# Performance work log

Hardware: AMD Instinct MI355X
Metric: run time of the kernel (lower is better)

## Reference

```python
import jax, jax.numpy as jnp
import numpy as np

B, N_SIDE, S = 64, 40, 512
N = N_SIDE * N_SIDE          # 1600 grid points (fl_feature_dims [1,40,40])
EMB = 10                     # embedding_dim
GDIM = 8                     # lie('homography').dim
WIDTH = 128
C1 = 20                      # first-layer output channels


def _embed(x, emb_dim):
    # sinusoidal embedding of each scalar coordinate: [..., D] -> [..., D*emb_dim]
    freqs = 2.0 ** jnp.arange(emb_dim // 2, dtype=x.dtype)
    ang = x[..., None] * freqs                       # [..., D, emb/2]
    e = jnp.concatenate([jnp.sin(ang), jnp.cos(ang)], axis=-1)  # [..., D, emb]
    return e.reshape(x.shape[:-1] + (x.shape[-1] * emb_dim,))


def _glorot(key, shape):
    fan_in = shape[0]
    return jax.random.normal(key, shape, dtype=jnp.float32) / np.sqrt(fan_in)


def setup_inputs() -> dict:
    key = jax.random.key(0)
    ks = jax.random.split(key, 16)
    inp = {
        'data':   jax.random.normal(ks[0], (B, N, 1), dtype=jnp.float32),
        'v0':     jax.random.normal(ks[1], (S, GDIM), dtype=jnp.float32),
        'v_last': jax.random.normal(ks[2], (S, GDIM), dtype=jnp.float32),
        # FirstLayer filter MLP: 2*EMB -> 20 -> 20 -> 1*C1
        'fl_w1': _glorot(ks[3], (2 * EMB, 20)), 'fl_b1': jnp.zeros((20,), jnp.float32),
        'fl_w2': _glorot(ks[4], (20, 20)),      'fl_b2': jnp.zeros((20,), jnp.float32),
        'fl_w3': _glorot(ks[5], (20, C1)),      'fl_b3': jnp.zeros((C1,), jnp.float32),
        # Hidden FilterMLP: EMB*GDIM=80 -> WIDTH -> C1*WIDTH
        's_w1': _glorot(ks[6], (EMB * GDIM, WIDTH)), 's_b1': jnp.zeros((WIDTH,), jnp.float32),
        's_w2': _glorot(ks[7], (WIDTH, C1 * WIDTH)), 's_b2': jnp.zeros((C1 * WIDTH,), jnp.float32),
        'fc1_w': _glorot(ks[8], (WIDTH, WIDTH)), 'fc1_b': jnp.zeros((WIDTH,), jnp.float32),
        'fc2_w': _glorot(ks[9], (WIDTH, WIDTH)), 'fc2_b': jnp.zeros((WIDTH,), jnp.float32),
        'pool_w': _glorot(ks[10], (WIDTH, 10)),  'pool_b': jnp.zeros((10,), jnp.float32),
    }
    return inp


def reference(data, v0, v_last, fl_w1, fl_b1, fl_w2, fl_b2, fl_w3, fl_b3,
              s_w1, s_b1, s_w2, s_b2, fc1_w, fc1_b, fc2_w, fc2_b, pool_w, pool_b):
    silu = jax.nn.silu
    # pixel grid in [-1,1]^2, homogeneous coords [N,3]
    lin = jnp.linspace(-1.0, 1.0, N_SIDE, dtype=data.dtype)
    xx, yy = jnp.meshgrid(lin, lin, indexing='ij')
    coords = jnp.stack([xx.ravel(), yy.ravel()], axis=-1)           # [N,2]
    xh = jnp.concatenate([coords, jnp.ones((N, 1), data.dtype)], -1)  # [N,3]
    # homography matrices: identity + small perturbation from 8 group params
    pert = jnp.concatenate([0.1 * v_last, jnp.zeros((S, 1), data.dtype)], -1).reshape(S, 3, 3)
    H = jnp.eye(3, dtype=data.dtype) + pert                          # [S,3,3]
    y = jnp.einsum('sij,nj->sni', H, xh)                             # [S,N,3]
    t = y[..., :2] / y[..., 2:3]                                     # projective action [S,N,2]
    # continuous-kernel first layer: filters generated by MLP on embedded coords
    e1 = _embed(t, EMB)                                              # [S,N,20]
    h = silu(e1 @ fl_w1 + fl_b1)
    h = silu(h @ fl_w2 + fl_b2)
    filt1 = h @ fl_w3 + fl_b3                                        # [S,N,C1]
    z = jnp.einsum('bn,sno->bso', data[:, :, 0], filt1) / N          # [B,S,C1]
    z = silu(z)
    # hidden FilterMLP on group samples v0 -> per-sample filters [S,C1,WIDTH]
    v0e = _embed(v0, EMB)                                            # [S,80]
    h2 = silu(v0e @ s_w1 + s_b1)                                     # [S,WIDTH]
    filt2 = (h2 @ s_w2 + s_b2).reshape(S, C1, WIDTH)
    # (1/S) * sum over group-sample and channel axes of broadcast product
    z = jnp.einsum('bsc,scw->bw', z, filt2) / S                      # [B,WIDTH]
    z = silu(z @ fc1_w + fc1_b) + z
    z = silu(z @ fc2_w + fc2_b) + z
    return z @ pool_w + pool_b                                       # [B,10]
```

## Files before the change

### kernel.cpp

```cpp
#include <hip/hip_runtime.h>

#define N_PTS 1600
#define NSIDE 40
#define SNUM  512
#define BNUM  64
#define C1D   20
#define WID   128

typedef _Float16 h8  __attribute__((ext_vector_type(8)));
typedef _Float16 h4  __attribute__((ext_vector_type(4)));
typedef __fp16   h2v __attribute__((ext_vector_type(2)));
typedef float    f4  __attribute__((ext_vector_type(4)));

__device__ __forceinline__ float silu_f(float x){
    return x * __builtin_amdgcn_rcpf(1.f + __expf(-x));
}
__device__ __forceinline__ void fma4(float4& a, float s, const float4 w){
    a.x += s*w.x; a.y += s*w.y; a.z += s*w.z; a.w += s*w.w;
}

__global__ __launch_bounds__(256) void ka_prep(
    const float* __restrict__ data, const float* __restrict__ v0,
    const float* __restrict__ s_w1, const float* __restrict__ s_b1,
    const float* __restrict__ s_w2, const float* __restrict__ s_b2,
    const float* __restrict__ w1, const float* __restrict__ b1,
    const float* __restrict__ w2, const float* __restrict__ b2,
    const float* __restrict__ w3, const float* __restrict__ b3,
    _Float16* __restrict__ dataA, float* __restrict__ f2g,
    _Float16* __restrict__ wPackA, float* __restrict__ bPackA,
    float* __restrict__ out2g)
{
    const int t  = threadIdx.x;
    const int bx = blockIdx.x;
    if (bx == 370) {
        const float* wsrc[3] = { w1, w2, w3 };
        const float* bsrc[3] = { b1, b2, b3 };
        for (int v = t; v < 3072; v += 256) {
            const int l = v >> 10, rem = v & 1023;
            const int cout = rem >> 5, cin = rem & 31;
            float x = 0.f;
            if (cout < 20 && cin < 20) x = wsrc[l][cin * 20 + cout];
            wPackA[v] = (_Float16)x;
        }
        if (t < 96) {
            const int l = t >> 5, cout = t & 31;
            bPackA[t] = (cout < 20) ? bsrc[l][cout] : 0.f;
        }
        for (int v = t; v < 8192; v += 256) out2g[v] = 0.f;
        return;
    }
    if (bx >= 320) {
        const int o  = (bx - 320) * 256 + t;
        const int L  = o & 63, cm = o >> 6;
        const int mt = cm & 3, ch = cm >> 2;
        const int b  = mt * 16 + (L & 15);
        const int nb = ch * 32 + (L >> 4) * 8;
        const float* src = data + b * N_PTS + nb;
        h8 v;
        #pragma unroll
        for (int j = 0; j < 8; j++) v[j] = (_Float16)src[j];
        *(h8*)(dataA + (size_t)o * 8) = v;
        return;
    }
    const int st  = bx / 10, ct = bx - st * 10;
    const int s0  = st * 16;
    const int col = ct * 256 + t;
    __shared__ __align__(16) float h2t[128][20];
    __shared__ __align__(16) float svt[16][8][10];

    if (t < 128) {
        const int ss = t >> 3, d = t & 7;
        const float val = v0[(s0 + ss) * 8 + d];
        float sv, cv;
        __sincosf(val, &sv, &cv);
        #pragma unroll
        for (int k = 0; k < 5; k++) {
            svt[ss][d][k]     = sv;
            svt[ss][d][5 + k] = cv;
            const float ns = 2.f * sv * cv;
            const float nc = 1.f - 2.f * sv * sv;
            sv = ns; cv = nc;
        }
    }
    __syncthreads();

    {
        const int j  = t & 127;
        const int sh = t >> 7;
        float hacc[8];
        const float bias1 = s_b1[j];
        #pragma unroll
        for (int u = 0; u < 8; u++) hacc[u] = bias1;
        for (int d = 0; d < 8; d++) {
            #pragma unroll
            for (int kk = 0; kk < 10; kk++) {
                const float wv = s_w1[(d * 10 + kk) * WID + j];
                #pragma unroll
                for (int u = 0; u < 8; u++)
                    hacc[u] += svt[sh * 8 + u][d][kk] * wv;
            }
        }
        #pragma unroll
        for (int u = 0; u < 8; u++) h2t[j][sh * 8 + u] = silu_f(hacc[u]);
    }
    __syncthreads();

    float4 acc[4];
    #pragma unroll
    for (int qq = 0; qq < 4; qq++) acc[qq] = make_float4(0.f, 0.f, 0.f, 0.f);
    #pragma unroll 4
    for (int i = 0; i < 128; i++) {
        const float wv = s_w2[i * 2560 + col];
        const float4* hh = (const float4*)&h2t[i][0];
        #pragma unroll
        for (int qq = 0; qq < 4; qq++) fma4(acc[qq], wv, hh[qq]);
    }
    const float bias = s_b2[col];
    const float* af = (const float*)acc;
    #pragma unroll
    for (int ss = 0; ss < 16; ss++)
        f2g[(s0 + ss) * 2560 + col] = af[ss] + bias;
}

__device__ __forceinline__ void embed_coord(
    int n, float hA, float hB, float hC, float h6, float h7, float h8c,
    h2v e5[5])
{
    const int i = n / NSIDE;
    const int j = n - i * NSIDE;
    const float x = -1.f + (float)i * (2.f/39.f);
    const float y = -1.f + (float)j * (2.f/39.f);
    const float yc = hA*x + hB*y + hC;
    const float y2 = h6*x + h7*y + h8c;
    const float tc = yc * __builtin_amdgcn_rcpf(y2);
    float e[10];
    float sv, cv;
    __sincosf(tc, &sv, &cv);
    #pragma unroll
    for (int k = 0; k < 5; k++) {
        e[k] = sv; e[5+k] = cv;
        const float ns = 2.f*sv*cv, nc = 1.f - 2.f*sv*sv; sv = ns; cv = nc;
    }
    #pragma unroll
    for (int k = 0; k < 5; k++)
        e5[k] = __builtin_amdgcn_cvt_pkrtz(e[2*k], e[2*k+1]);
}

#define ASTRIDE 40

__global__ __launch_bounds__(512, 8) void k1_filt_z(
    const _Float16* __restrict__ dataA, const float* __restrict__ v_last,
    const _Float16* __restrict__ wPackA, const float* __restrict__ bPackA,
    float* __restrict__ zpart)
{
    const int s    = blockIdx.x & 511;
    const int half = blockIdx.x >> 9;
    const int nb0  = half * 800;
    const int t    = threadIdx.x;
    const int lane = t & 63;
    const int w    = t >> 6;
    const int q    = lane >> 4;
    const int l15  = lane & 15;
    const int mtbase = (w & 1) * 2;
    const int kcs    = w >> 1;
    const int ep   = lane >> 1;
    const int ec   = lane & 1;
    const int erow = w*16 + ep + ((ep >> 4) * 112);

    __shared__ __align__(16) unsigned char pool[21504];
    __shared__ __align__(16) _Float16 filtB[20 * 264];
    __shared__ __align__(16) _Float16 wlds[3072];
    __shared__ __align__(16) float    blds[96];
    _Float16* act = (_Float16*)pool;
    float*    red = (float*)pool;

    for (int v = t; v < 1536; v += 512)
        ((unsigned int*)wlds)[v] = ((const unsigned int*)wPackA)[v];
    if (t < 96) blds[t] = bPackA[t];

    float Hm[9];
    #pragma unroll
    for (int k = 0; k < 9; k++) Hm[k] = (k == 0 || k == 4 || k == 8) ? 1.f : 0.f;
    #pragma unroll
    for (int k = 0; k < 8; k++) Hm[k] += 0.1f * v_last[s*8 + k];
    const float hA = ec ? Hm[3] : Hm[0];
    const float hB = ec ? Hm[4] : Hm[1];
    const float hC = ec ? Hm[5] : Hm[2];

    f4 zacc[2][2];
    #pragma unroll
    for (int mi = 0; mi < 2; mi++) { zacc[mi][0] = (f4)(0.f); zacc[mi][1] = (f4)(0.f); }
    const f4 zero4 = (f4)(0.f);

    if (ec == 0) {
        unsigned long long* pz = (unsigned long long*)(act + erow*ASTRIDE + 20);
        pz[0] = 0ull; pz[1] = 0ull; pz[2] = 0ull;
    }

    __syncthreads();

    for (int base = 0; base < 800; base += 256) {
        const int tn = min(256, 800 - base);

        if (erow < tn) {
            h2v e5[5];
            embed_coord(nb0 + base + erow, hA, hB, hC, Hm[6], Hm[7], Hm[8], e5);
            #pragma unroll
            for (int k = 0; k < 5; k++)
                *(h2v*)(act + erow*ASTRIDE + ec*10 + 2*k) = e5[k];
        }

        const int nmt = tn >> 4;
        #pragma unroll
        for (int l = 0; l < 3; l++) {
            const h8 wf0 = *(const h8*)(wlds + ((l*2+0)*16 + l15) * 32 + q*8);
            const h8 wf1 = *(const h8*)(wlds + ((l*2+1)*16 + l15) * 32 + q*8);
            const float b0 = blds[(l*2+0)*16 + l15];
            const float b1 = blds[(l*2+1)*16 + l15];
            for (int mt = w; mt < nmt; mt += 8) {
                const int r0 = mt * 16;
                const h8 af = *(const h8*)(act + (r0 + l15)*ASTRIDE + q*8);
                f4 D0 = __builtin_amdgcn_mfma_f32_16x16x32_f16(af, wf0, zero4, 0, 0, 0);
                f4 D1 = __builtin_amdgcn_mfma_f32_16x16x32_f16(af, wf1, zero4, 0, 0, 0);
                if (l < 2) {
                    #pragma unroll
                    for (int r = 0; r < 4; r++) {
                        const int p = r0 + q*4 + r;
                        act[p*ASTRIDE + l15] = (_Float16)silu_f(D0[r] + b0);
                        if (l15 < 4)
                            act[p*ASTRIDE + 16 + l15] = (_Float16)silu_f(D1[r] + b1);
                    }
                } else {
                    h4 p0, p1;
                    #pragma unroll
                    for (int r = 0; r < 4; r++) {
                        p0[r] = (_Float16)(D0[r] + b0);
                        p1[r] = (_Float16)(D1[r] + b1);
                    }
                    *(h4*)(filtB + l15*264 + r0 + q*4) = p0;
                    if (l15 < 4)
                        *(h4*)(filtB + (16 + l15)*264 + r0 + q*4) = p1;
                }
            }
        }
        __syncthreads();

        const int nkc = tn >> 5;
        const int r1row = (l15 < 4) ? (16 + l15) : 0;
        #pragma unroll
        for (int kk = 0; kk < 2; kk++) {
            const int kc = kcs + kk*4;
            if (kc < nkc) {
                const int gchunk = ((nb0 + base) >> 5) + kc;
                const h8 bf0 = *(const h8*)(filtB + l15  *264 + kc*32 + q*8);
                const h8 bf1 = *(const h8*)(filtB + r1row*264 + kc*32 + q*8);
                #pragma unroll
                for (int mi = 0; mi < 2; mi++) {
                    const int mt = mtbase + mi;
                    const h8 afz = *(const h8*)(dataA + ((size_t)(gchunk*4 + mt)*64 + lane)*8);
                    zacc[mi][0] = __builtin_amdgcn_mfma_f32_16x16x32_f16(afz, bf0, zacc[mi][0], 0, 0, 0);
                    zacc[mi][1] = __builtin_amdgcn_mfma_f32_16x16x32_f16(afz, bf1, zacc[mi][1], 0, 0, 0);
                }
            }
        }
        __syncthreads();
    }

    #pragma unroll
    for (int mi = 0; mi < 2; mi++) {
        #pragma unroll
        for (int r = 0; r < 4; r++) {
            const int bl = mi*16 + q*4 + r;
            red[(w*32 + bl)*21 + l15] = zacc[mi][0][r];
            if (l15 < 4) red[(w*32 + bl)*21 + 16 + l15] = zacc[mi][1][r];
        }
    }
    __syncthreads();
    for (int v = t; v < 1280; v += 512) {
        const int c = v >> 6, b = v & 63;
        const int mts = b >> 5, bl = b & 31;
        const float sum = red[((mts    )*32 + bl)*21 + c]
                        + red[((mts + 2)*32 + bl)*21 + c]
                        + red[((mts + 4)*32 + bl)*21 + c]
                        + red[((mts + 6)*32 + bl)*21 + c];
        zpart[(half*512 + s)*1280 + v] = sum;
    }
}

__global__ __launch_bounds__(256) void k2_contract(
    const float* __restrict__ zg, const float* __restrict__ f2g,
    float* __restrict__ out2g)
{
    const int blk = blockIdx.x;
    const int sg  = blk >> 1;
    const int wh  = blk & 1;
    const int s0  = sg * 4;
    const int w0  = wh * 64;
    const int t   = threadIdx.x;
    __shared__ __align__(16) float zl[4*1280];
    __shared__ __align__(16) float fl[4*20*64];
    #pragma unroll
    for (int sp = 0; sp < 4; sp++) {
        const int srow = (s0 + sp) * 1280;
        for (int r = t; r < 1280; r += 256) {
            const float a0 = zg[srow + r];
            const float a1 = zg[512*1280 + srow + r];
            zl[sp*1280 + r] = silu_f((a0 + a1) * (1.f / (float)N_PTS));
        }
        for (int u = t; u < 1280; u += 256) {
            const int c = u >> 6, ww = u & 63;
            fl[sp*1280 + u] = f2g[(s0 + sp)*2560 + c*128 + w0 + ww];
        }
    }
    __syncthreads();
    const int ww = t & 63, bh = t >> 6;
    float4 acc[4];
    #pragma unroll
    for (int qq = 0; qq < 4; qq++) acc[qq] = make_float4(0.f, 0.f, 0.f, 0.f);
    #pragma unroll 4
    for (int sc = 0; sc < 80; sc++) {
        const float f = fl[sc * 64 + ww];
        const float4* zz = (const float4*)&zl[sc * 64 + bh * 16];
        #pragma unroll
        for (int qq = 0; qq < 4; qq++) fma4(acc[qq], f, zz[qq]);
    }
    const float* af = (const float*)acc;
    #pragma unroll
    for (int idx = 0; idx < 16; idx++) {
        const int b = bh * 16 + idx;
        atomicAdd(&out2g[b * 128 + w0 + ww], af[idx]);
    }
}

__global__ __launch_bounds__(128) void k3_tail(
    const float* __restrict__ out2g,
    const float* __restrict__ fc1w, const float* __restrict__ fc1b,
    const float* __restrict__ fc2w, const float* __restrict__ fc2b,
    const float* __restrict__ pw,   const float* __restrict__ pb,
    float* __restrict__ out)
{
    const int b = blockIdx.x, t = threadIdx.x;
    __shared__ float zb[128], r1[128], r2[128];
    zb[t] = out2g[b * 128 + t] * (1.f / (float)SNUM);
    __syncthreads();
    float a = fc1b[t];
    #pragma unroll 8
    for (int i = 0; i < 128; i++) a += zb[i] * fc1w[i * 128 + t];
    r1[t] = silu_f(a) + zb[t];
    __syncthreads();
    a = fc2b[t];
    #pragma unroll 8
    for (int i = 0; i < 128; i++) a += r1[i] * fc2w[i * 128 + t];
    r2[t] = silu_f(a) + r1[t];
    __syncthreads();
    if (t < 10) {
        float o = pb[t];
        #pragma unroll 8
        for (int i = 0; i < 128; i++) o += r2[i] * pw[i * 10 + t];
        out[b * 10 + t] = o;
    }
}

extern "C" void kernel_launch(void* const* d_in, const int* in_sizes, int n_in,
                              void* d_out, int out_size, void* d_ws, size_t ws_size,
                              hipStream_t stream) {
    const float* data   = (const float*)d_in[0];
    const float* v0     = (const float*)d_in[1];
    const float* v_last = (const float*)d_in[2];
    const float* fl_w1  = (const float*)d_in[3];
    const float* fl_b1  = (const float*)d_in[4];
    const float* fl_w2  = (const float*)d_in[5];
    const float* fl_b2  = (const float*)d_in[6];
    const float* fl_w3  = (const float*)d_in[7];
    const float* fl_b3  = (const float*)d_in[8];
    const float* s_w1   = (const float*)d_in[9];
    const float* s_b1   = (const float*)d_in[10];
    const float* s_w2   = (const float*)d_in[11];
    const float* s_b2   = (const float*)d_in[12];
    const float* fc1_w  = (const float*)d_in[13];
    const float* fc1_b  = (const float*)d_in[14];
    const float* fc2_w  = (const float*)d_in[15];
    const float* fc2_b  = (const float*)d_in[16];
    const float* pool_w = (const float*)d_in[17];
    const float* pool_b = (const float*)d_in[18];
    float* out = (float*)d_out;

    float* ws        = (float*)d_ws;
    _Float16* dataA  = (_Float16*)ws;
    float* zpart  = ws    + 51200;
    float* f2g    = zpart + 1310720;
    float* out2g  = f2g   + 1310720;
    _Float16* wPackA = (_Float16*)(out2g + 8192);
    float* bPackA = out2g + 8192 + 1536;

    ka_prep    <<<371, 256, 0, stream>>>(data, v0, s_w1, s_b1, s_w2, s_b2,
                                         fl_w1, fl_b1, fl_w2, fl_b2, fl_w3, fl_b3,
                                         dataA, f2g, wPackA, bPackA, out2g);
    k1_filt_z  <<<1024, 512, 0, stream>>>(dataA, v_last, wPackA, bPackA, zpart);
    k2_contract<<<256, 256, 0, stream>>>(zpart, f2g, out2g);
    k3_tail    <<<64, 128, 0, stream>>>(out2g, fc1_w, fc1_b, fc2_w, fc2_b,
                                        pool_w, pool_b, out);
}
```

Baseline: 181.7 us.

## Split fused filter+GEMM kernel into separate filter and z-GEMM kernels; halve prep tile

The fused kernel that generated the first-layer filters and immediately contracted them with the data is split in two. A filter-generation kernel writes fp16 filters to global memory, and a separate 256-thread GEMM kernel reads them back to compute the partial z sums. Removing the LDS filter staging and the barriers inside the loop should let each kernel reach better occupancy and a simpler schedule. In exchange it adds a round trip of about 32 MB of fp16 filters through global memory and one extra kernel launch. The prep kernel also now processes 8 group samples per block instead of 16, doubling its block count for more parallelism.

```diff
diff --git a/kernel.cpp b/kernel.cpp
--- a/kernel.cpp
+++ b/kernel.cpp
@@ -32,7 +32,7 @@
 {
     const int t  = threadIdx.x;
     const int bx = blockIdx.x;
-    if (bx == 370) {
+    if (bx == 690) {
         const float* wsrc[3] = { w1, w2, w3 };
         const float* bsrc[3] = { b1, b2, b3 };
         for (int v = t; v < 3072; v += 256) {
@@ -49,8 +49,8 @@
         for (int v = t; v < 8192; v += 256) out2g[v] = 0.f;
         return;
     }
-    if (bx >= 320) {
-        const int o  = (bx - 320) * 256 + t;
+    if (bx >= 640) {
+        const int o  = (bx - 640) * 256 + t;
         const int L  = o & 63, cm = o >> 6;
         const int mt = cm & 3, ch = cm >> 2;
         const int b  = mt * 16 + (L & 15);
@@ -63,12 +63,12 @@
         return;
     }
     const int st  = bx / 10, ct = bx - st * 10;
-    const int s0  = st * 16;
+    const int s0  = st * 8;
     const int col = ct * 256 + t;
-    __shared__ __align__(16) float h2t[128][20];
-    __shared__ __align__(16) float svt[16][8][10];
-
-    if (t < 128) {
+    __shared__ __align__(16) float h2t[128][12];
+    __shared__ __align__(16) float svt[8][8][10];
+
+    if (t < 64) {
         const int ss = t >> 3, d = t & 7;
         const float val = v0[(s0 + ss) * 8 + d];
         float sv, cv;
@@ -87,38 +87,38 @@
     {
         const int j  = t & 127;
         const int sh = t >> 7;
-        float hacc[8];
+        float hacc[4];
         const float bias1 = s_b1[j];
         #pragma unroll
-        for (int u = 0; u < 8; u++) hacc[u] = bias1;
+        for (int u = 0; u < 4; u++) hacc[u] = bias1;
         for (int d = 0; d < 8; d++) {
             #pragma unroll
             for (int kk = 0; kk < 10; kk++) {
                 const float wv = s_w1[(d * 10 + kk) * WID + j];
                 #pragma unroll
-                for (int u = 0; u < 8; u++)
-                    hacc[u] += svt[sh * 8 + u][d][kk] * wv;
+                for (int u = 0; u < 4; u++)
+                    hacc[u] += svt[sh * 4 + u][d][kk] * wv;
             }
         }
         #pragma unroll
-        for (int u = 0; u < 8; u++) h2t[j][sh * 8 + u] = silu_f(hacc[u]);
-    }
-    __syncthreads();
-
-    float4 acc[4];
-    #pragma unroll
-    for (int qq = 0; qq < 4; qq++) acc[qq] = make_float4(0.f, 0.f, 0.f, 0.f);
+        for (int u = 0; u < 4; u++) h2t[j][sh * 4 + u] = silu_f(hacc[u]);
+    }
+    __syncthreads();
+
+    float4 acc[2];
+    acc[0] = make_float4(0.f, 0.f, 0.f, 0.f);
+    acc[1] = make_float4(0.f, 0.f, 0.f, 0.f);
     #pragma unroll 4
     for (int i = 0; i < 128; i++) {
         const float wv = s_w2[i * 2560 + col];
         const float4* hh = (const float4*)&h2t[i][0];
-        #pragma unroll
-        for (int qq = 0; qq < 4; qq++) fma4(acc[qq], wv, hh[qq]);
+        fma4(acc[0], wv, hh[0]);
+        fma4(acc[1], wv, hh[1]);
     }
     const float bias = s_b2[col];
     const float* af = (const float*)acc;
     #pragma unroll
-    for (int ss = 0; ss < 16; ss++)
+    for (int ss = 0; ss < 8; ss++)
         f2g[(s0 + ss) * 2560 + col] = af[ss] + bias;
 }
 
@@ -148,10 +148,10 @@
 
 #define ASTRIDE 40
 
-__global__ __launch_bounds__(512, 8) void k1_filt_z(
-    const _Float16* __restrict__ dataA, const float* __restrict__ v_last,
+__global__ __launch_bounds__(512, 8) void kf_filt(
+    const float* __restrict__ v_last,
     const _Float16* __restrict__ wPackA, const float* __restrict__ bPackA,
-    float* __restrict__ zpart)
+    _Float16* __restrict__ filtG)
 {
     const int s    = blockIdx.x & 511;
     const int half = blockIdx.x >> 9;
@@ -161,18 +161,13 @@
     const int w    = t >> 6;
     const int q    = lane >> 4;
     const int l15  = lane & 15;
-    const int mtbase = (w & 1) * 2;
-    const int kcs    = w >> 1;
     const int ep   = lane >> 1;
     const int ec   = lane & 1;
     const int erow = w*16 + ep + ((ep >> 4) * 112);
 
-    __shared__ __align__(16) unsigned char pool[21504];
-    __shared__ __align__(16) _Float16 filtB[20 * 264];
+    __shared__ __align__(16) _Float16 act[256 * ASTRIDE];
     __shared__ __align__(16) _Float16 wlds[3072];
     __shared__ __align__(16) float    blds[96];
-    _Float16* act = (_Float16*)pool;
-    float*    red = (float*)pool;
 
     for (int v = t; v < 1536; v += 512)
         ((unsigned int*)wlds)[v] = ((const unsigned int*)wPackA)[v];
@@ -187,17 +182,14 @@
     const float hB = ec ? Hm[4] : Hm[1];
     const float hC = ec ? Hm[5] : Hm[2];
 
-    f4 zacc[2][2];
-    #pragma unroll
-    for (int mi = 0; mi < 2; mi++) { zacc[mi][0] = (f4)(0.f); zacc[mi][1] = (f4)(0.f); }
-    const f4 zero4 = (f4)(0.f);
-
     if (ec == 0) {
         unsigned long long* pz = (unsigned long long*)(act + erow*ASTRIDE + 20);
         pz[0] = 0ull; pz[1] = 0ull; pz[2] = 0ull;
     }
 
     __syncthreads();
+
+    _Float16* fgs = filtG + (size_t)(half*512 + s) * 16000;
 
     for (int base = 0; base < 800; base += 256) {
         const int tn = min(256, 800 - base);
@@ -217,6 +209,7 @@
             const h8 wf1 = *(const h8*)(wlds + ((l*2+1)*16 + l15) * 32 + q*8);
             const float b0 = blds[(l*2+0)*16 + l15];
             const float b1 = blds[(l*2+1)*16 + l15];
+            const f4 zero4 = (f4)(0.f);
             for (int mt = w; mt < nmt; mt += 8) {
                 const int r0 = mt * 16;
                 const h8 af = *(const h8*)(act + (r0 + l15)*ASTRIDE + q*8);
@@ -237,52 +230,62 @@
                         p0[r] = (_Float16)(D0[r] + b0);
                         p1[r] = (_Float16)(D1[r] + b1);
                     }
-                    *(h4*)(filtB + l15*264 + r0 + q*4) = p0;
+                    *(h4*)(fgs + l15*800 + base + r0 + q*4) = p0;
                     if (l15 < 4)
-                        *(h4*)(filtB + (16 + l15)*264 + r0 + q*4) = p1;
+                        *(h4*)(fgs + (16 + l15)*800 + base + r0 + q*4) = p1;
                 }
             }
         }
-        __syncthreads();
-
-        const int nkc = tn >> 5;
-        const int r1row = (l15 < 4) ? (16 + l15) : 0;
-        #pragma unroll
-        for (int kk = 0; kk < 2; kk++) {
-            const int kc = kcs + kk*4;
-            if (kc < nkc) {
-                const int gchunk = ((nb0 + base) >> 5) + kc;
-                const h8 bf0 = *(const h8*)(filtB + l15  *264 + kc*32 + q*8);
-                const h8 bf1 = *(const h8*)(filtB + r1row*264 + kc*32 + q*8);
-                #pragma unroll
-                for (int mi = 0; mi < 2; mi++) {
-                    const int mt = mtbase + mi;
-                    const h8 afz = *(const h8*)(dataA + ((size_t)(gchunk*4 + mt)*64 + lane)*8);
-                    zacc[mi][0] = __builtin_amdgcn_mfma_f32_16x16x32_f16(afz, bf0, zacc[mi][0], 0, 0, 0);
-                    zacc[mi][1] = __builtin_amdgcn_mfma_f32_16x16x32_f16(afz, bf1, zacc[mi][1], 0, 0, 0);
-                }
-            }
-        }
-        __syncthreads();
-    }
-
-    #pragma unroll
-    for (int mi = 0; mi < 2; mi++) {
+    }
+}
+
+__global__ __launch_bounds__(256, 6) void kz_gemm(
+    const _Float16* __restrict__ dataA, const _Float16* __restrict__ filtG,
+    float* __restrict__ zpart)
+{
+    const int s    = blockIdx.x & 511;
+    const int half = blockIdx.x >> 9;
+    const int t    = threadIdx.x;
+    const int lane = t & 63;
+    const int w    = t >> 6;
+    const int q    = lane >> 4;
+    const int l15  = lane & 15;
+
+    __shared__ __align__(16) float red[4 * 64 * 21];
+
+    const _Float16* fgs = filtG + (size_t)(half*512 + s) * 16000;
+    const int r1row = (l15 < 4) ? (16 + l15) : 0;
+
+    f4 zacc[4][2];
+    #pragma unroll
+    for (int mt = 0; mt < 4; mt++) { zacc[mt][0] = (f4)(0.f); zacc[mt][1] = (f4)(0.f); }
+
+    for (int kc = w; kc < 25; kc += 4) {
+        const h8 bf0 = *(const h8*)(fgs + l15  *800 + kc*32 + q*8);
+        const h8 bf1 = *(const h8*)(fgs + r1row*800 + kc*32 + q*8);
+        const int gchunk = half*25 + kc;
+        #pragma unroll
+        for (int mt = 0; mt < 4; mt++) {
+            const h8 afz = *(const h8*)(dataA + ((size_t)(gchunk*4 + mt)*64 + lane)*8);
+            zacc[mt][0] = __builtin_amdgcn_mfma_f32_16x16x32_f16(afz, bf0, zacc[mt][0], 0, 0, 0);
+            zacc[mt][1] = __builtin_amdgcn_mfma_f32_16x16x32_f16(afz, bf1, zacc[mt][1], 0, 0, 0);
+        }
+    }
+
+    #pragma unroll
+    for (int mt = 0; mt < 4; mt++) {
         #pragma unroll
         for (int r = 0; r < 4; r++) {
-            const int bl = mi*16 + q*4 + r;
-            red[(w*32 + bl)*21 + l15] = zacc[mi][0][r];
-            if (l15 < 4) red[(w*32 + bl)*21 + 16 + l15] = zacc[mi][1][r];
-        }
-    }
-    __syncthreads();
-    for (int v = t; v < 1280; v += 512) {
+            const int b = mt*16 + q*4 + r;
+            red[(w*64 + b)*21 + l15] = zacc[mt][0][r];
+            if (l15 < 4) red[(w*64 + b)*21 + 16 + l15] = zacc[mt][1][r];
+        }
+    }
+    __syncthreads();
+    for (int v = t; v < 1280; v += 256) {
         const int c = v >> 6, b = v & 63;
-        const int mts = b >> 5, bl = b & 31;
-        const float sum = red[((mts    )*32 + bl)*21 + c]
-                        + red[((mts + 2)*32 + bl)*21 + c]
-                        + red[((mts + 4)*32 + bl)*21 + c]
-                        + red[((mts + 6)*32 + bl)*21 + c];
+        const float sum = red[(      b)*21 + c] + red[( 64 + b)*21 + c]
+                        + red[(128 + b)*21 + c] + red[(192 + b)*21 + c];
         zpart[(half*512 + s)*1280 + v] = sum;
     }
 }
@@ -392,11 +395,13 @@
     float* out2g  = f2g   + 1310720;
     _Float16* wPackA = (_Float16*)(out2g + 8192);
     float* bPackA = out2g + 8192 + 1536;
-
-    ka_prep    <<<371, 256, 0, stream>>>(data, v0, s_w1, s_b1, s_w2, s_b2,
+    _Float16* filtG = (_Float16*)(bPackA + 96);
+
+    ka_prep    <<<691, 256, 0, stream>>>(data, v0, s_w1, s_b1, s_w2, s_b2,
                                          fl_w1, fl_b1, fl_w2, fl_b2, fl_w3, fl_b3,
                                          dataA, f2g, wPackA, bPackA, out2g);
-    k1_filt_z  <<<1024, 512, 0, stream>>>(dataA, v_last, wPackA, bPackA, zpart);
+    kf_filt    <<<1024, 512, 0, stream>>>(v_last, wPackA, bPackA, filtG);
+    kz_gemm    <<<1024, 256, 0, stream>>>(dataA, filtG, zpart);
     k2_contract<<<256, 256, 0, stream>>>(zpart, f2g, out2g);
     k3_tail    <<<64, 128, 0, stream>>>(out2g, fc1_w, fc1_b, fc2_w, fc2_b,
                                         pool_w, pool_b, out);
```

Result: no change. 180.2 us (-0.8%).
